# Performance work log

Measured on AMD Instinct MI355X. Metric: run time of the kernel, lower is better.

Reference implementation:

```python
import jax, jax.numpy as jnp
import numpy as np

# config constants (match init_kwargs)
T, B = 32, 32
H, W_IN, C_IN = 128, 128, 2
FH, FW = 32, 32
CF, CP = 64, 32
OUT = 128
PATCH = 8
TOPK_R = 4
KWTA = 16
SPARSITY = 0.5
BETA = 0.9
VTH = 1.0
EVT = 0.5
PH, PW = H // PATCH, W_IN // PATCH  # 16,16


def _topk_mask(x, k):
    # mask of entries >= k-th largest along last axis
    k = min(k, x.shape[-1])
    if k <= 0:
        return jnp.zeros_like(x)
    top_vals = jax.lax.top_k(x, k)[0]
    thresh = top_vals[..., k - 1:k]
    return (x >= thresh).astype(x.dtype)


def _block_sparse_mask(w, sparsity, block=4):
    h, wk, cin, cout = w.shape
    bh, bw = h // block, wk // block
    if bh == 0 or bw == 0:
        # 3x3 kernel with block=4 degenerates to a dense (all-ones) mask
        return jnp.ones((h, wk, 1, 1), dtype=w.dtype)
    core = w[:bh * block, :bw * block, :, :]
    blocks = core.reshape(bh, block, bw, block, cin, cout)
    scores = jnp.mean(jnp.abs(blocks), axis=(1, 3, 4, 5)).reshape(-1)
    keep = max(1, int(scores.shape[0] * (1.0 - sparsity)))
    gate = _topk_mask(scores[None, :], keep).reshape(bh, bw)
    gate = jnp.repeat(jnp.repeat(gate, block, axis=0), block, axis=1)
    mask = jnp.ones((h, wk), dtype=w.dtype).at[:bh * block, :bw * block].set(gate)
    return mask[:, :, None, None]


def _conv(x, w):
    return jax.lax.conv_general_dilated(
        x, w, (1, 1), 'SAME', dimension_numbers=('NHWC', 'HWIO', 'NHWC'))


@jax.custom_vjp
def _spike(v):
    return (v > 0).astype(v.dtype)

def _spike_fwd(v):
    return _spike(v), v

def _spike_bwd(v, g):
    # superspike surrogate gradient (k=25)
    return (g / (1.0 + 25.0 * jnp.abs(v)) ** 2,)

_spike.defvjp(_spike_fwd, _spike_bwd)


def setup_inputs() -> dict:
    key = jax.random.key(0)
    ks = jax.random.split(key, 8)
    def vs_uniform(k, shape):
        # VarianceScaling(1.0, fan_avg, uniform)
        fan_in = shape[0] * shape[1] * shape[2] if len(shape) == 4 else shape[0]
        fan_out = shape[0] * shape[1] * shape[3] if len(shape) == 4 else shape[1]
        limit = float(np.sqrt(3.0 / ((fan_in + fan_out) / 2.0)))
        return jax.random.uniform(k, shape, jnp.float32, -limit, limit)
    return {
        'x_seq': jax.random.normal(ks[0], (T, B, H, W_IN, C_IN), jnp.float32),
        'w_fovea': vs_uniform(ks[1], (3, 3, C_IN, CF)),
        'w_periph': vs_uniform(ks[2], (3, 3, C_IN, CP)),
        'head_w': vs_uniform(ks[3], (CF + CP, OUT)),
        'head_b': jnp.zeros((OUT,), jnp.float32),
        'route_w': vs_uniform(ks[4], (PH * PW, OUT)),
        'route_b': jnp.zeros((OUT,), jnp.float32),
    }


def reference(x_seq, w_fovea, w_periph, head_w, head_b, route_w, route_b):
    # block-sparse masks are constant across time: apply once
    w_f = w_fovea * _block_sparse_mask(w_fovea, SPARSITY)
    w_p = w_periph * _block_sparse_mask(w_periph, SPARSITY)

    def step(carry, x_t):
        vf, vp = carry
        event_mask = (jnp.abs(x_t) > EVT).astype(x_t.dtype)
        xs = x_t * event_mask
        # region activation router: mean |x| per patch
        patches = xs.reshape(B, PH, PATCH, PW, PATCH, C_IN)
        scores = jnp.mean(jnp.abs(patches), axis=(2, 4, 5)).reshape(B, PH * PW)
        region_gate = _topk_mask(scores, TOPK_R)
        # foveal crop around the best patch
        best = jnp.argmax(scores, axis=-1)
        cy = best // PW * PATCH + PATCH // 2
        cx = best % PW * PATCH + PATCH // 2
        y0 = jnp.clip(cy - FH // 2, 0, H - FH)
        x0 = jnp.clip(cx - FW // 2, 0, W_IN - FW)
        fovea = jax.vmap(
            lambda img, y, x: jax.lax.dynamic_slice(img, (y, x, 0), (FH, FW, C_IN))
        )(xs, y0, x0)
        # fovea conv + k-WTA channel gate
        ff = _conv(fovea, w_f)
        sal = jnp.mean(jnp.abs(ff), axis=(1, 2))            # (B, CF)
        channel_gate = _topk_mask(sal, KWTA)
        ff = ff * channel_gate[:, None, None, :]
        # periphery: half-res linear resize + conv
        periph = jax.image.resize(xs, (B, H // 2, W_IN // 2, C_IN), method='linear')
        pf = _conv(periph, w_p)
        # LIF updates (beta decay, threshold, soft reset)
        vf = BETA * vf + ff
        sf = _spike(vf - VTH)
        vf = vf - sf * VTH
        vp = BETA * vp + pf
        sp = _spike(vp - VTH)
        vp = vp - sp * VTH
        fused = jnp.concatenate([jnp.mean(sf, axis=(1, 2)), jnp.mean(sp, axis=(1, 2))], axis=-1)
        logits_t = fused @ head_w + head_b + scores @ route_w + route_b
        sr_t = jnp.stack([jnp.mean(sf), jnp.mean(sp)])
        active_ratio = jnp.mean(event_mask)
        route_stats = jnp.mean(region_gate, axis=0)
        chan_stats = jnp.mean(channel_gate, axis=0)
        return (vf, vp), (logits_t, sr_t, active_ratio, route_stats, chan_stats)

    vf0 = jnp.zeros((B, FH, FW, CF), x_seq.dtype)
    vp0 = jnp.zeros((B, H // 2, W_IN // 2, CP), x_seq.dtype)
    _, (logits_seq, sr_seq, active_seq, route_seq, chan_seq) = jax.lax.scan(
        step, (vf0, vp0), x_seq)
    out = jnp.mean(logits_seq, axis=0)  # readout='mean'
    return (out, logits_seq, jnp.mean(sr_seq, axis=0), jnp.mean(active_seq),
            jnp.mean(route_seq, axis=0), jnp.mean(chan_seq, axis=0))
```

## Files before the change

### kernel.cpp

```cpp
#include <hip/hip_runtime.h>

#define T_ 32
#define B_ 32
#define H_ 128
#define W_ 128
#define C_ 2
#define NP_ 256
#define CF_ 64
#define CP_ 32
#define OUT_ 128

#define PROW 136
#define PTB  8976
#define WTB  2312

#define OFF_LOGITS 4096
#define OFF_SR     135168
#define OFF_ACTIVE 135170
#define OFF_ROUTE  135171
#define OFF_CHAN   135427

#define CNT_N 323

typedef float f2 __attribute__((ext_vector_type(2)));

__device__ __forceinline__ float f4c(const float4& v, int i) {
  switch (i & 3) { case 0: return v.x; case 1: return v.y; case 2: return v.z; default: return v.w; }
}

__global__ void __launch_bounds__(256) k_pre(const float* __restrict__ x,
    const float* __restrict__ wf,
    float* __restrict__ scores_g, float* __restrict__ P, float* __restrict__ Wfbuf,
    float* __restrict__ chan_gate, unsigned* __restrict__ cnts) {
  const int tb = blockIdx.x, tid = threadIdx.x;
  __shared__ __align__(16) float xt[34*256];
  __shared__ float sm[NP_];
  __shared__ float salred[256];
  __shared__ float salv[64];
  __shared__ unsigned wsum[4];
  __shared__ int2 syx;
  const float* img = x + (size_t)tb*32768;
  unsigned cnt = 0;
  for (int chunk = 0; chunk < 4; ++chunk) {
    const int r0 = chunk*16;
    __syncthreads();
    for (int i4 = tid; i4 < 34*64; i4 += 256) {
      const int rr = i4 >> 6, off4 = i4 & 63;
      const int xr = 2*r0 - 1 + rr;
      float4 vv = make_float4(0.f, 0.f, 0.f, 0.f);
      if (xr >= 0 && xr < H_) {
        vv = *reinterpret_cast<const float4*>(img + (size_t)xr*256 + off4*4);
        if (rr >= 1 && rr <= 32) {
          cnt += (fabsf(vv.x) > 0.5f) + (fabsf(vv.y) > 0.5f)
               + (fabsf(vv.z) > 0.5f) + (fabsf(vv.w) > 0.5f);
        }
        vv.x = (fabsf(vv.x) > 0.5f) ? vv.x : 0.f;
        vv.y = (fabsf(vv.y) > 0.5f) ? vv.y : 0.f;
        vv.z = (fabsf(vv.z) > 0.5f) ? vv.z : 0.f;
        vv.w = (fabsf(vv.w) > 0.5f) ? vv.w : 0.f;
      }
      *reinterpret_cast<float4*>(&xt[i4*4]) = vv;
    }
    __syncthreads();
    {
      const int patch = tid >> 2, q = tid & 3;
      const int prl = patch >> 4, pc = patch & 15;
      const int row = 1 + prl*8 + q*2;
      float s = 0.f;
#pragma unroll
      for (int r2 = 0; r2 < 2; ++r2)
#pragma unroll
        for (int j = 0; j < 4; ++j) {
          const float4 vv = *reinterpret_cast<const float4*>(&xt[(row + r2)*256 + pc*16 + j*4]);
          s += fabsf(vv.x) + fabsf(vv.y) + fabsf(vv.z) + fabsf(vv.w);
        }
      s += __shfl_down(s, 1);
      s += __shfl_down(s, 2);
      if (q == 0) {
        const float sv = s * (1.f/128.f);
        sm[chunk*64 + patch] = sv;
        scores_g[tb*NP_ + chunk*64 + patch] = sv;
      }
    }
    float* Pt = P + (size_t)tb * PTB;
    if (tid < 128) {
      const int r = tid >> 3, rem = tid & 7;
      const int px4 = rem >> 1, ci = rem & 1;
      const int px = (px4 < 2) ? (px4 - 2) : (62 + px4);
      Pt[(r0 + r + 1)*PROW + (px + 2)*2 + ci] = 0.f;
    }
    if (chunk == 0 && tid < PROW) Pt[tid] = 0.f;
    if (chunk == 3 && tid < PROW) Pt[65*PROW + tid] = 0.f;
#pragma unroll
    for (int k = 0; k < 8; ++k) {
      const int idx = k*256 + tid;
      const int ci = idx & 1, rest = idx >> 1;
      const int col = rest & 63, row16 = rest >> 6;
      const int pr = r0 + row16;
      float wy0=0.125f, wy1=0.375f, wy2=0.375f, wy3=0.125f;
      if (pr == 0)       { wy0=0.f;     wy1=3.f/7.f; wy2=3.f/7.f; wy3=1.f/7.f; }
      else if (pr == 63) { wy0=1.f/7.f; wy1=3.f/7.f; wy2=3.f/7.f; wy3=0.f; }
      float wx0=0.125f, wx1=0.375f, wx2=0.375f, wx3=0.125f;
      if (col == 0)       { wx0=0.f;     wx1=3.f/7.f; wx2=3.f/7.f; wx3=1.f/7.f; }
      else if (col == 63) { wx0=1.f/7.f; wx1=3.f/7.f; wx2=3.f/7.f; wx3=0.f; }
      const int lr = 2*row16;
      const int cc0 = 2*col - 1;
      float val = 0.f;
#pragma unroll
      for (int j = 0; j < 4; ++j) {
        const float wyj = (j==0)?wy0:(j==1)?wy1:(j==2)?wy2:wy3;
        float h = 0.f;
#pragma unroll
        for (int i = 0; i < 4; ++i) {
          const float wxi = (i==0)?wx0:(i==1)?wx1:(i==2)?wx2:wx3;
          int cc = cc0 + i; cc = cc < 0 ? 0 : (cc > W_-1 ? W_-1 : cc);
          h += wxi * xt[(lr + j)*256 + cc*2 + ci];
        }
        val += wyj * h;
      }
      Pt[(pr + 1)*PROW + (col + 2)*2 + ci] = val;
    }
  }
  unsigned c64 = cnt;
#pragma unroll
  for (int off = 32; off > 0; off >>= 1) c64 += __shfl_down(c64, off);
  if ((tid & 63) == 0) wsum[tid >> 6] = c64;
  __syncthreads();
  if (tid == 0) atomicAdd(&cnts[0], wsum[0] + wsum[1] + wsum[2] + wsum[3]);
  {
    const float v = sm[tid];
    int cg = 0, eqb = 0;
    for (int q = 0; q < NP_; ++q) {
      cg  += (sm[q] > v) ? 1 : 0;
      eqb += ((sm[q] == v) && (q < tid)) ? 1 : 0;
    }
    if (cg < 4) atomicAdd(&cnts[1 + tid], 1u);
    if (cg == 0 && eqb == 0) {
      const int cy = (tid >> 4)*8 + 4, cx = (tid & 15)*8 + 4;
      int y0 = cy - 16; y0 = y0 < 0 ? 0 : (y0 > 96 ? 96 : y0);
      int x0 = cx - 16; x0 = x0 < 0 ? 0 : (x0 > 96 ? 96 : x0);
      syx = make_int2(y0, x0);
    }
  }
  float* tile = xt;
  for (int i = tid; i < 34*68; i += 256) tile[i] = 0.f;
  __syncthreads();
  const int2 yx = syx;
  {
    const int row = tid >> 3, seg = tid & 7;
    const float* src = img + (size_t)(yx.x + row)*256 + (yx.y + seg*4)*2;
    float4 a = *reinterpret_cast<const float4*>(src);
    float4 b4 = *reinterpret_cast<const float4*>(src + 4);
    a.x  = (fabsf(a.x)  > 0.5f) ? a.x  : 0.f;
    a.y  = (fabsf(a.y)  > 0.5f) ? a.y  : 0.f;
    a.z  = (fabsf(a.z)  > 0.5f) ? a.z  : 0.f;
    a.w  = (fabsf(a.w)  > 0.5f) ? a.w  : 0.f;
    b4.x = (fabsf(b4.x) > 0.5f) ? b4.x : 0.f;
    b4.y = (fabsf(b4.y) > 0.5f) ? b4.y : 0.f;
    b4.z = (fabsf(b4.z) > 0.5f) ? b4.z : 0.f;
    b4.w = (fabsf(b4.w) > 0.5f) ? b4.w : 0.f;
    float* dst = &tile[(row + 1)*68 + (seg*4 + 1)*2];
    *reinterpret_cast<float2*>(dst)     = make_float2(a.x, a.y);
    *reinterpret_cast<float2*>(dst + 2) = make_float2(a.z, a.w);
    *reinterpret_cast<float2*>(dst + 4) = make_float2(b4.x, b4.y);
    *reinterpret_cast<float2*>(dst + 6) = make_float2(b4.z, b4.w);
  }
  __syncthreads();
  {
    float* dst = Wfbuf + (size_t)tb*WTB;
    for (int i = tid; i < WTB/4; i += 256)
      *reinterpret_cast<float4*>(dst + i*4) = *reinterpret_cast<const float4*>(&tile[i*4]);
  }
  const int c = tid & 63, xg = tid >> 6;
  float wreg[18];
#pragma unroll
  for (int k = 0; k < 18; ++k) wreg[k] = wf[k*CF_ + c];
  const float* tbase = &tile[xg*16];
  float4 wb[3][5];
#pragma unroll
  for (int m = 0; m < 5; ++m) {
    wb[0][m] = *reinterpret_cast<const float4*>(tbase + m*4);
    wb[1][m] = *reinterpret_cast<const float4*>(tbase + 68 + m*4);
  }
  float sal = 0.f;
#pragma unroll
  for (int yy = 0; yy < 32; ++yy) {
#pragma unroll
    for (int m = 0; m < 5; ++m)
      wb[(yy+2)%3][m] = *reinterpret_cast<const float4*>(tbase + (yy+2)*68 + m*4);
#pragma unroll
    for (int k = 0; k < 8; ++k) {
      float acc = 0.f;
#pragma unroll
      for (int dy = 0; dy < 3; ++dy) {
#pragma unroll
        for (int dx = 0; dx < 3; ++dx) {
          const int r = k + dx;
          const float4 f = wb[(yy+dy)%3][r >> 1];
          acc += f4c(f, (r&1)*2)     * wreg[(dy*3+dx)*2]
               + f4c(f, (r&1)*2 + 1) * wreg[(dy*3+dx)*2 + 1];
        }
      }
      sal += fabsf(acc);
    }
  }
  salred[tid] = sal;
  __syncthreads();
  if (tid < 64)
    salv[tid] = (salred[tid] + salred[64+tid] + salred[128+tid] + salred[192+tid]) * (1.f/1024.f);
  __syncthreads();
  if (tid < 64) {
    const float sv = salv[tid];
    int cg = 0;
    for (int q = 0; q < 64; ++q) cg += (salv[q] > sv) ? 1 : 0;
    const float gate = (cg < 16) ? 1.f : 0.f;
    chan_gate[tb*CF_ + tid] = gate;
    if (gate > 0.f) atomicAdd(&cnts[257 + tid], 1u);
  }
}

__global__ void __launch_bounds__(256, 4) k_mem(const float* __restrict__ Wfbuf,
    const float* __restrict__ P, const float* __restrict__ wf, const float* __restrict__ wp,
    const float* __restrict__ chan_gate,
    unsigned* __restrict__ fov_part, unsigned* __restrict__ per_part) {
  const int tid = threadIdx.x;
  const int w = tid >> 6, l = tid & 63;
  if (blockIdx.x < 2048) {
    const int blk = blockIdx.x;
    const int b = blk >> 6, rem = blk & 63, cp = rem >> 1, half = rem & 1;
    const int ch0 = cp*2;
    const int row = half*16 + w*4 + (l >> 4);
    const int px0 = (l & 15)*2;
    f2 w01[18];
#pragma unroll
    for (int k = 0; k < 18; ++k) {
      f2 t_; t_.x = wf[k*CF_ + ch0]; t_.y = wf[k*CF_ + ch0 + 1];
      w01[k] = t_;
    }
    const float* p0 = Wfbuf + (size_t)b*WTB + (size_t)row*68 + px0*2;
    const float* gp = chan_gate + b*CF_ + ch0;
    const unsigned obase = (unsigned)((b*32 + cp)*8 + half*4 + w);
    f2 va = (f2)0.f, vb = (f2)0.f;
    float4 A[6], Bv[6];
    f2 gA, gB;
#pragma unroll
    for (int dy = 0; dy < 3; ++dy) {
      A[2*dy]   = *reinterpret_cast<const float4*>(p0 + dy*68);
      A[2*dy+1] = *reinterpret_cast<const float4*>(p0 + dy*68 + 4);
    }
    gA.x = gp[0]; gA.y = gp[1];
    for (int t = 0; t < T_; t += 2) {
      {
        const float* p1 = p0 + (size_t)(t + 1)*(B_*WTB);
#pragma unroll
        for (int dy = 0; dy < 3; ++dy) {
          Bv[2*dy]   = *reinterpret_cast<const float4*>(p1 + dy*68);
          Bv[2*dy+1] = *reinterpret_cast<const float4*>(p1 + dy*68 + 4);
        }
        gB.x = gp[(t + 1)*B_*CF_]; gB.y = gp[(t + 1)*B_*CF_ + 1];
      }
      {
        f2 aa = (f2)0.f, ab = (f2)0.f;
#pragma unroll
        for (int dy = 0; dy < 3; ++dy) {
          const float4 fa = A[2*dy], fb = A[2*dy+1];
          const f2 w0 = w01[dy*6], w0y = w01[dy*6+1], w1 = w01[dy*6+2],
                   w1y = w01[dy*6+3], w2 = w01[dy*6+4], w2y = w01[dy*6+5];
          aa += fa.x*w0 + fa.y*w0y + fa.z*w1 + fa.w*w1y + fb.x*w2 + fb.y*w2y;
          ab += fa.z*w0 + fa.w*w0y + fb.x*w1 + fb.y*w1y + fb.z*w2 + fb.w*w2y;
        }
        f2 na = 0.9f*va + aa*gA;
        f2 nb = 0.9f*vb + ab*gA;
        const bool s0a = na.x > 1.f, s1a = na.y > 1.f, s0b = nb.x > 1.f, s1b = nb.y > 1.f;
        va.x = s0a ? na.x - 1.f : na.x;  va.y = s1a ? na.y - 1.f : na.y;
        vb.x = s0b ? nb.x - 1.f : nb.x;  vb.y = s1b ? nb.y - 1.f : nb.y;
        const unsigned packed =
            (unsigned)(__popcll(__ballot(s0a)) + __popcll(__ballot(s0b)))
          | ((unsigned)(__popcll(__ballot(s1a)) + __popcll(__ballot(s1b))) << 16);
        if (l == 0) fov_part[obase + (unsigned)t*8192u] = packed;
      }
      if (t + 2 < T_) {
        const float* p2 = p0 + (size_t)(t + 2)*(B_*WTB);
#pragma unroll
        for (int dy = 0; dy < 3; ++dy) {
          A[2*dy]   = *reinterpret_cast<const float4*>(p2 + dy*68);
          A[2*dy+1] = *reinterpret_cast<const float4*>(p2 + dy*68 + 4);
        }
        gA.x = gp[(t + 2)*B_*CF_]; gA.y = gp[(t + 2)*B_*CF_ + 1];
      }
      {
        f2 aa = (f2)0.f, ab = (f2)0.f;
#pragma unroll
        for (int dy = 0; dy < 3; ++dy) {
          const float4 fa = Bv[2*dy], fb = Bv[2*dy+1];
          const f2 w0 = w01[dy*6], w0y = w01[dy*6+1], w1 = w01[dy*6+2],
                   w1y = w01[dy*6+3], w2 = w01[dy*6+4], w2y = w01[dy*6+5];
          aa += fa.x*w0 + fa.y*w0y + fa.z*w1 + fa.w*w1y + fb.x*w2 + fb.y*w2y;
          ab += fa.z*w0 + fa.w*w0y + fb.x*w1 + fb.y*w1y + fb.z*w2 + fb.w*w2y;
        }
        f2 na = 0.9f*va + aa*gB;
        f2 nb = 0.9f*vb + ab*gB;
        const bool s0a = na.x > 1.f, s1a = na.y > 1.f, s0b = nb.x > 1.f, s1b = nb.y > 1.f;
        va.x = s0a ? na.x - 1.f : na.x;  va.y = s1a ? na.y - 1.f : na.y;
        vb.x = s0b ? nb.x - 1.f : nb.x;  vb.y = s1b ? nb.y - 1.f : nb.y;
        const unsigned packed =
            (unsigned)(__popcll(__ballot(s0a)) + __popcll(__ballot(s0b)))
          | ((unsigned)(__popcll(__ballot(s1a)) + __popcll(__ballot(s1b))) << 16);
        if (l == 0) fov_part[obase + (unsigned)(t + 1)*8192u] = packed;
      }
    }
  } else {
    const int blk = blockIdx.x - 2048;
    const int b = blk >> 7, rem = blk & 127, cp = rem >> 3, rq = rem & 7;
    const int ch0 = cp*2;
    const int row = rq*8 + w*2 + (l >> 5);
    const int px0 = (l & 31)*2;
    f2 w01[18];
#pragma unroll
    for (int k = 0; k < 18; ++k) {
      f2 t_; t_.x = wp[k*CP_ + ch0]; t_.y = wp[k*CP_ + ch0 + 1];
      w01[k] = t_;
    }
    const float* p0 = P + (size_t)b*PTB + (size_t)row*PROW + px0*2;
    const unsigned obase = (unsigned)((b*16 + cp)*32 + rq*4 + w);
    f2 va = (f2)0.f, vb = (f2)0.f;
    float4 A[9], Bv[9];
#pragma unroll
    for (int dy = 0; dy < 3; ++dy) {
      A[3*dy]   = *reinterpret_cast<const float4*>(p0 + dy*PROW);
      A[3*dy+1] = *reinterpret_cast<const float4*>(p0 + dy*PROW + 4);
      A[3*dy+2] = *reinterpret_cast<const float4*>(p0 + dy*PROW + 8);
    }
    for (int t = 0; t < T_; t += 2) {
      {
        const float* p1 = p0 + (size_t)(t + 1)*PTB*B_;
#pragma unroll
        for (int dy = 0; dy < 3; ++dy) {
          Bv[3*dy]   = *reinterpret_cast<const float4*>(p1 + dy*PROW);
          Bv[3*dy+1] = *reinterpret_cast<const float4*>(p1 + dy*PROW + 4);
          Bv[3*dy+2] = *reinterpret_cast<const float4*>(p1 + dy*PROW + 8);
        }
      }
      {
        f2 aa = (f2)0.f, ab = (f2)0.f;
#pragma unroll
        for (int dy = 0; dy < 3; ++dy) {
          const float4 f0 = A[3*dy], f1 = A[3*dy+1], f2v = A[3*dy+2];
          const f2 w0 = w01[dy*6], w0y = w01[dy*6+1], w1 = w01[dy*6+2],
                   w1y = w01[dy*6+3], w2 = w01[dy*6+4], w2y = w01[dy*6+5];
          aa += f0.z*w0 + f0.w*w0y + f1.x*w1 + f1.y*w1y + f1.z*w2 + f1.w*w2y;
          ab += f1.x*w0 + f1.y*w0y + f1.z*w1 + f1.w*w1y + f2v.x*w2 + f2v.y*w2y;
        }
        f2 na = 0.9f*va + aa;
        f2 nb = 0.9f*vb + ab;
        const bool s0a = na.x > 1.f, s1a = na.y > 1.f, s0b = nb.x > 1.f, s1b = nb.y > 1.f;
        va.x = s0a ? na.x - 1.f : na.x;  va.y = s1a ? na.y - 1.f : na.y;
        vb.x = s0b ? nb.x - 1.f : nb.x;  vb.y = s1b ? nb.y - 1.f : nb.y;
        const unsigned packed =
            (unsigned)(__popcll(__ballot(s0a)) + __popcll(__ballot(s0b)))
          | ((unsigned)(__popcll(__ballot(s1a)) + __popcll(__ballot(s1b))) << 16);
        if (l == 0) per_part[obase + (unsigned)t*16384u] = packed;
      }
      if (t + 2 < T_) {
        const float* p2 = p0 + (size_t)(t + 2)*PTB*B_;
#pragma unroll
        for (int dy = 0; dy < 3; ++dy) {
          A[3*dy]   = *reinterpret_cast<const float4*>(p2 + dy*PROW);
          A[3*dy+1] = *reinterpret_cast<const float4*>(p2 + dy*PROW + 4);
          A[3*dy+2] = *reinterpret_cast<const float4*>(p2 + dy*PROW + 8);
        }
      }
      {
        f2 aa = (f2)0.f, ab = (f2)0.f;
#pragma unroll
        for (int dy = 0; dy < 3; ++dy) {
          const float4 f0 = Bv[3*dy], f1 = Bv[3*dy+1], f2v = Bv[3*dy+2];
          const f2 w0 = w01[dy*6], w0y = w01[dy*6+1], w1 = w01[dy*6+2],
                   w1y = w01[dy*6+3], w2 = w01[dy*6+4], w2y = w01[dy*6+5];
          aa += f0.z*w0 + f0.w*w0y + f1.x*w1 + f1.y*w1y + f1.z*w2 + f1.w*w2y;
          ab += f1.x*w0 + f1.y*w0y + f1.z*w1 + f1.w*w1y + f2v.x*w2 + f2v.y*w2y;
        }
        f2 na = 0.9f*va + aa;
        f2 nb = 0.9f*vb + ab;
        const bool s0a = na.x > 1.f, s1a = na.y > 1.f, s0b = nb.x > 1.f, s1b = nb.y > 1.f;
        va.x = s0a ? na.x - 1.f : na.x;  va.y = s1a ? na.y - 1.f : na.y;
        vb.x = s0b ? nb.x - 1.f : nb.x;  vb.y = s1b ? nb.y - 1.f : nb.y;
        const unsigned packed =
            (unsigned)(__popcll(__ballot(s0a)) + __popcll(__ballot(s0b)))
          | ((unsigned)(__popcll(__ballot(s1a)) + __popcll(__ballot(s1b))) << 16);
        if (l == 0) per_part[obase + (unsigned)(t + 1)*16384u] = packed;
      }
    }
  }
}

__global__ void __launch_bounds__(256) k_logits(const float* __restrict__ scores,
    const unsigned* __restrict__ fov_part, const unsigned* __restrict__ per_part,
    const float* __restrict__ head_w, const float* __restrict__ head_b,
    const float* __restrict__ route_w, const float* __restrict__ route_b,
    float* __restrict__ logits, unsigned* __restrict__ tot) {
  const int tb = blockIdx.x, tid = threadIdx.x;
  __shared__ float sc[NP_];
  __shared__ float fu[96];
  sc[tid] = scores[tb*NP_ + tid];
  if (tid < 64) {
    const unsigned* fp = fov_part + (size_t)tb*256;
    const int cp = tid >> 1, sh = (tid & 1)*16;
    unsigned fsum = 0;
#pragma unroll
    for (int i = 0; i < 8; ++i) fsum += (fp[cp*8 + i] >> sh) & 0xFFFFu;
    fu[tid] = (float)fsum * (1.f/1024.f);
    unsigned r = fsum;
#pragma unroll
    for (int off = 32; off > 0; off >>= 1) r += __shfl_down(r, off);
    if (tid == 0) atomicAdd(&tot[0], r);
  } else if (tid < 128) {
    const int c = tid - 64;
    unsigned psum = 0;
    if (c < 32) {
      const unsigned* pp = per_part + (size_t)tb*512;
      const int cp = c >> 1, sh = (c & 1)*16;
#pragma unroll 8
      for (int i = 0; i < 32; ++i) psum += (pp[cp*32 + i] >> sh) & 0xFFFFu;
      fu[64 + c] = (float)psum * (1.f/4096.f);
    }
    unsigned r = psum;
#pragma unroll
    for (int off = 32; off > 0; off >>= 1) r += __shfl_down(r, off);
    if (tid == 64) atomicAdd(&tot[1], r);
  }
  __syncthreads();
  if (tid < 128) {
    const int o = tid;
    float acc = head_b[o] + route_b[o];
#pragma unroll 8
    for (int k = 0; k < 96; ++k)  acc += fu[k]*head_w[k*OUT_ + o];
#pragma unroll 8
    for (int p = 0; p < NP_; ++p) acc += sc[p]*route_w[p*OUT_ + o];
    logits[tb*OUT_ + o] = acc;
  }
}

__global__ void __launch_bounds__(256) k_final(const float* __restrict__ logits,
    float* __restrict__ dout, const unsigned* __restrict__ cnts) {
  const int blk = blockIdx.x, tid = threadIdx.x;
  if (blk < 16) {
    const int idx = blk*256 + tid;
    const int b = idx >> 7, o = idx & 127;
    float s = 0.f;
#pragma unroll
    for (int t = 0; t < T_; ++t) s += logits[(t*B_ + b)*OUT_ + o];
    dout[idx] = s * (1.f/32.f);
  } else {
    if (tid == 0) {
      dout[OFF_SR]     = (float)cnts[321] * (1.f/67108864.f);
      dout[OFF_SR + 1] = (float)cnts[322] * (1.f/134217728.f);
      dout[OFF_ACTIVE] = (float)cnts[0]   * (1.f/33554432.f);
    }
    dout[OFF_ROUTE + tid] = (float)cnts[1 + tid] * (1.f/1024.f);
    if (tid < 64) dout[OFF_CHAN + tid] = (float)cnts[257 + tid] * (1.f/1024.f);
  }
}

extern "C" void kernel_launch(void* const* d_in, const int* in_sizes, int n_in,
                              void* d_out, int out_size, void* d_ws, size_t ws_size,
                              hipStream_t stream) {
  const float* x       = (const float*)d_in[0];
  const float* wf      = (const float*)d_in[1];
  const float* wp      = (const float*)d_in[2];
  const float* head_w  = (const float*)d_in[3];
  const float* head_b  = (const float*)d_in[4];
  const float* route_w = (const float*)d_in[5];
  const float* route_b = (const float*)d_in[6];
  float* out = (float*)d_out;

  float*    ws_P      = (float*)d_ws;
  float*    ws_Wf     = ws_P + (size_t)1024*PTB;
  float*    ws_scores = ws_Wf + (size_t)1024*WTB;
  float*    ws_gate   = ws_scores + T_*B_*NP_;
  unsigned* fov_part  = (unsigned*)(ws_gate + T_*B_*CF_);
  unsigned* per_part  = fov_part + (size_t)T_*B_*256;
  unsigned* ws_cnt    = per_part + (size_t)T_*B_*512;

  hipMemsetAsync(ws_cnt, 0, CNT_N*sizeof(unsigned), stream);

  k_pre   <<<T_*B_, 256, 0, stream>>>(x, wf, ws_scores, ws_P, ws_Wf, ws_gate, ws_cnt);
  k_mem   <<<6144,  256, 0, stream>>>(ws_Wf, ws_P, wf, wp, ws_gate, fov_part, per_part);
  k_logits<<<T_*B_, 256, 0, stream>>>(ws_scores, fov_part, per_part, head_w, head_b,
                                      route_w, route_b, out + OFF_LOGITS, ws_cnt + 321);
  k_final <<<17, 256, 0, stream>>>(out + OFF_LOGITS, out, ws_cnt);
}
```

Baseline: 272.5 us.

## Stage conv input tiles in double-buffered LDS instead of per-thread global loads

The fovea and periphery LIF conv loops in k_mem now load each timestep's input tile cooperatively into a double-buffered shared-memory array. Previously every thread fetched its own overlapping 3-row stencil straight from global memory. The next timestep is prefetched into registers and written to the other LDS buffer after compute, with one barrier per step. This removes redundant global loads of overlapping halo rows, at the cost of a __syncthreads per timestep and about 10.9 KB of LDS per block, which could limit occupancy.

```diff
diff --git a/kernel.cpp b/kernel.cpp
--- a/kernel.cpp
+++ b/kernel.cpp
@@ -223,173 +223,123 @@
     const float* __restrict__ P, const float* __restrict__ wf, const float* __restrict__ wp,
     const float* __restrict__ chan_gate,
     unsigned* __restrict__ fov_part, unsigned* __restrict__ per_part) {
+  __shared__ __align__(16) float lds[2*1360];
   const int tid = threadIdx.x;
   const int w = tid >> 6, l = tid & 63;
   if (blockIdx.x < 2048) {
     const int blk = blockIdx.x;
     const int b = blk >> 6, rem = blk & 63, cp = rem >> 1, half = rem & 1;
     const int ch0 = cp*2;
-    const int row = half*16 + w*4 + (l >> 4);
-    const int px0 = (l & 15)*2;
+    const int brow = w*4 + (l >> 4);
+    const int po = (l & 15)*4;
     f2 w01[18];
 #pragma unroll
     for (int k = 0; k < 18; ++k) {
       f2 t_; t_.x = wf[k*CF_ + ch0]; t_.y = wf[k*CF_ + ch0 + 1];
       w01[k] = t_;
     }
-    const float* p0 = Wfbuf + (size_t)b*WTB + (size_t)row*68 + px0*2;
+    const float* gsrc = Wfbuf + (size_t)b*WTB + half*16*68;
     const float* gp = chan_gate + b*CF_ + ch0;
     const unsigned obase = (unsigned)((b*32 + cp)*8 + half*4 + w);
     f2 va = (f2)0.f, vb = (f2)0.f;
-    float4 A[6], Bv[6];
-    f2 gA, gB;
-#pragma unroll
-    for (int dy = 0; dy < 3; ++dy) {
-      A[2*dy]   = *reinterpret_cast<const float4*>(p0 + dy*68);
-      A[2*dy+1] = *reinterpret_cast<const float4*>(p0 + dy*68 + 4);
-    }
-    gA.x = gp[0]; gA.y = gp[1];
-    for (int t = 0; t < T_; t += 2) {
-      {
-        const float* p1 = p0 + (size_t)(t + 1)*(B_*WTB);
-#pragma unroll
-        for (int dy = 0; dy < 3; ++dy) {
-          Bv[2*dy]   = *reinterpret_cast<const float4*>(p1 + dy*68);
-          Bv[2*dy+1] = *reinterpret_cast<const float4*>(p1 + dy*68 + 4);
-        }
-        gB.x = gp[(t + 1)*B_*CF_]; gB.y = gp[(t + 1)*B_*CF_ + 1];
-      }
-      {
-        f2 aa = (f2)0.f, ab = (f2)0.f;
-#pragma unroll
-        for (int dy = 0; dy < 3; ++dy) {
-          const float4 fa = A[2*dy], fb = A[2*dy+1];
-          const f2 w0 = w01[dy*6], w0y = w01[dy*6+1], w1 = w01[dy*6+2],
-                   w1y = w01[dy*6+3], w2 = w01[dy*6+4], w2y = w01[dy*6+5];
-          aa += fa.x*w0 + fa.y*w0y + fa.z*w1 + fa.w*w1y + fb.x*w2 + fb.y*w2y;
-          ab += fa.z*w0 + fa.w*w0y + fb.x*w1 + fb.y*w1y + fb.z*w2 + fb.w*w2y;
-        }
-        f2 na = 0.9f*va + aa*gA;
-        f2 nb = 0.9f*vb + ab*gA;
-        const bool s0a = na.x > 1.f, s1a = na.y > 1.f, s0b = nb.x > 1.f, s1b = nb.y > 1.f;
-        va.x = s0a ? na.x - 1.f : na.x;  va.y = s1a ? na.y - 1.f : na.y;
-        vb.x = s0b ? nb.x - 1.f : nb.x;  vb.y = s1b ? nb.y - 1.f : nb.y;
-        const unsigned packed =
-            (unsigned)(__popcll(__ballot(s0a)) + __popcll(__ballot(s0b)))
-          | ((unsigned)(__popcll(__ballot(s1a)) + __popcll(__ballot(s1b))) << 16);
-        if (l == 0) fov_part[obase + (unsigned)t*8192u] = packed;
-      }
-      if (t + 2 < T_) {
-        const float* p2 = p0 + (size_t)(t + 2)*(B_*WTB);
-#pragma unroll
-        for (int dy = 0; dy < 3; ++dy) {
-          A[2*dy]   = *reinterpret_cast<const float4*>(p2 + dy*68);
-          A[2*dy+1] = *reinterpret_cast<const float4*>(p2 + dy*68 + 4);
-        }
-        gA.x = gp[(t + 2)*B_*CF_]; gA.y = gp[(t + 2)*B_*CF_ + 1];
-      }
-      {
-        f2 aa = (f2)0.f, ab = (f2)0.f;
-#pragma unroll
-        for (int dy = 0; dy < 3; ++dy) {
-          const float4 fa = Bv[2*dy], fb = Bv[2*dy+1];
-          const f2 w0 = w01[dy*6], w0y = w01[dy*6+1], w1 = w01[dy*6+2],
-                   w1y = w01[dy*6+3], w2 = w01[dy*6+4], w2y = w01[dy*6+5];
-          aa += fa.x*w0 + fa.y*w0y + fa.z*w1 + fa.w*w1y + fb.x*w2 + fb.y*w2y;
-          ab += fa.z*w0 + fa.w*w0y + fb.x*w1 + fb.y*w1y + fb.z*w2 + fb.w*w2y;
-        }
-        f2 na = 0.9f*va + aa*gB;
-        f2 nb = 0.9f*vb + ab*gB;
-        const bool s0a = na.x > 1.f, s1a = na.y > 1.f, s0b = nb.x > 1.f, s1b = nb.y > 1.f;
-        va.x = s0a ? na.x - 1.f : na.x;  va.y = s1a ? na.y - 1.f : na.y;
-        vb.x = s0b ? nb.x - 1.f : nb.x;  vb.y = s1b ? nb.y - 1.f : nb.y;
-        const unsigned packed =
-            (unsigned)(__popcll(__ballot(s0a)) + __popcll(__ballot(s0b)))
-          | ((unsigned)(__popcll(__ballot(s1a)) + __popcll(__ballot(s1b))) << 16);
-        if (l == 0) fov_part[obase + (unsigned)(t + 1)*8192u] = packed;
-      }
+    float4 r0, r1;
+    r0 = *reinterpret_cast<const float4*>(gsrc + tid*4);
+    if (tid < 50) r1 = *reinterpret_cast<const float4*>(gsrc + (tid + 256)*4);
+    *reinterpret_cast<float4*>(&lds[tid*4]) = r0;
+    if (tid < 50) *reinterpret_cast<float4*>(&lds[(tid + 256)*4]) = r1;
+    int cur = 0;
+    for (int t = 0; t < T_; ++t) {
+      __syncthreads();
+      if (t + 1 < T_) {
+        const float* gn = gsrc + (size_t)(t + 1)*(B_*WTB);
+        r0 = *reinterpret_cast<const float4*>(gn + tid*4);
+        if (tid < 50) r1 = *reinterpret_cast<const float4*>(gn + (tid + 256)*4);
+      }
+      __builtin_amdgcn_sched_barrier(0);
+      f2 g; g.x = gp[(size_t)t*B_*CF_]; g.y = gp[(size_t)t*B_*CF_ + 1];
+      const float* Lb = &lds[cur*1360];
+      f2 aa = (f2)0.f, ab = (f2)0.f;
+#pragma unroll
+      for (int dy = 0; dy < 3; ++dy) {
+        const float4 fa = *reinterpret_cast<const float4*>(Lb + (brow + dy)*68 + po);
+        const float4 fb = *reinterpret_cast<const float4*>(Lb + (brow + dy)*68 + po + 4);
+        const f2 w0 = w01[dy*6], w0y = w01[dy*6+1], w1 = w01[dy*6+2],
+                 w1y = w01[dy*6+3], w2 = w01[dy*6+4], w2y = w01[dy*6+5];
+        aa += fa.x*w0 + fa.y*w0y + fa.z*w1 + fa.w*w1y + fb.x*w2 + fb.y*w2y;
+        ab += fa.z*w0 + fa.w*w0y + fb.x*w1 + fb.y*w1y + fb.z*w2 + fb.w*w2y;
+      }
+      f2 na = 0.9f*va + aa*g;
+      f2 nb = 0.9f*vb + ab*g;
+      const bool s0a = na.x > 1.f, s1a = na.y > 1.f, s0b = nb.x > 1.f, s1b = nb.y > 1.f;
+      va.x = s0a ? na.x - 1.f : na.x;  va.y = s1a ? na.y - 1.f : na.y;
+      vb.x = s0b ? nb.x - 1.f : nb.x;  vb.y = s1b ? nb.y - 1.f : nb.y;
+      const unsigned packed =
+          (unsigned)(__popcll(__ballot(s0a)) + __popcll(__ballot(s0b)))
+        | ((unsigned)(__popcll(__ballot(s1a)) + __popcll(__ballot(s1b))) << 16);
+      if (l == 0) fov_part[obase + (unsigned)t*8192u] = packed;
+      if (t + 1 < T_) {
+        float* Lw = &lds[(cur ^ 1)*1360];
+        *reinterpret_cast<float4*>(Lw + tid*4) = r0;
+        if (tid < 50) *reinterpret_cast<float4*>(Lw + (tid + 256)*4) = r1;
+      }
+      cur ^= 1;
     }
   } else {
     const int blk = blockIdx.x - 2048;
     const int b = blk >> 7, rem = blk & 127, cp = rem >> 3, rq = rem & 7;
     const int ch0 = cp*2;
-    const int row = rq*8 + w*2 + (l >> 5);
-    const int px0 = (l & 31)*2;
+    const int brow = w*2 + (l >> 5);
+    const int po = (l & 31)*4;
     f2 w01[18];
 #pragma unroll
     for (int k = 0; k < 18; ++k) {
       f2 t_; t_.x = wp[k*CP_ + ch0]; t_.y = wp[k*CP_ + ch0 + 1];
       w01[k] = t_;
     }
-    const float* p0 = P + (size_t)b*PTB + (size_t)row*PROW + px0*2;
+    const float* gsrc = P + (size_t)b*PTB + rq*8*PROW;
     const unsigned obase = (unsigned)((b*16 + cp)*32 + rq*4 + w);
     f2 va = (f2)0.f, vb = (f2)0.f;
-    float4 A[9], Bv[9];
-#pragma unroll
-    for (int dy = 0; dy < 3; ++dy) {
-      A[3*dy]   = *reinterpret_cast<const float4*>(p0 + dy*PROW);
-      A[3*dy+1] = *reinterpret_cast<const float4*>(p0 + dy*PROW + 4);
-      A[3*dy+2] = *reinterpret_cast<const float4*>(p0 + dy*PROW + 8);
-    }
-    for (int t = 0; t < T_; t += 2) {
-      {
-        const float* p1 = p0 + (size_t)(t + 1)*PTB*B_;
-#pragma unroll
-        for (int dy = 0; dy < 3; ++dy) {
-          Bv[3*dy]   = *reinterpret_cast<const float4*>(p1 + dy*PROW);
-          Bv[3*dy+1] = *reinterpret_cast<const float4*>(p1 + dy*PROW + 4);
-          Bv[3*dy+2] = *reinterpret_cast<const float4*>(p1 + dy*PROW + 8);
-        }
-      }
-      {
-        f2 aa = (f2)0.f, ab = (f2)0.f;
-#pragma unroll
-        for (int dy = 0; dy < 3; ++dy) {
-          const float4 f0 = A[3*dy], f1 = A[3*dy+1], f2v = A[3*dy+2];
-          const f2 w0 = w01[dy*6], w0y = w01[dy*6+1], w1 = w01[dy*6+2],
-                   w1y = w01[dy*6+3], w2 = w01[dy*6+4], w2y = w01[dy*6+5];
-          aa += f0.z*w0 + f0.w*w0y + f1.x*w1 + f1.y*w1y + f1.z*w2 + f1.w*w2y;
-          ab += f1.x*w0 + f1.y*w0y + f1.z*w1 + f1.w*w1y + f2v.x*w2 + f2v.y*w2y;
-        }
-        f2 na = 0.9f*va + aa;
-        f2 nb = 0.9f*vb + ab;
-        const bool s0a = na.x > 1.f, s1a = na.y > 1.f, s0b = nb.x > 1.f, s1b = nb.y > 1.f;
-        va.x = s0a ? na.x - 1.f : na.x;  va.y = s1a ? na.y - 1.f : na.y;
-        vb.x = s0b ? nb.x - 1.f : nb.x;  vb.y = s1b ? nb.y - 1.f : nb.y;
-        const unsigned packed =
-            (unsigned)(__popcll(__ballot(s0a)) + __popcll(__ballot(s0b)))
-          | ((unsigned)(__popcll(__ballot(s1a)) + __popcll(__ballot(s1b))) << 16);
-        if (l == 0) per_part[obase + (unsigned)t*16384u] = packed;
-      }
-      if (t + 2 < T_) {
-        const float* p2 = p0 + (size_t)(t + 2)*PTB*B_;
-#pragma unroll
-        for (int dy = 0; dy < 3; ++dy) {
-          A[3*dy]   = *reinterpret_cast<const float4*>(p2 + dy*PROW);
-          A[3*dy+1] = *reinterpret_cast<const float4*>(p2 + dy*PROW + 4);
-          A[3*dy+2] = *reinterpret_cast<const float4*>(p2 + dy*PROW + 8);
-        }
-      }
-      {
-        f2 aa = (f2)0.f, ab = (f2)0.f;
-#pragma unroll
-        for (int dy = 0; dy < 3; ++dy) {
-          const float4 f0 = Bv[3*dy], f1 = Bv[3*dy+1], f2v = Bv[3*dy+2];
-          const f2 w0 = w01[dy*6], w0y = w01[dy*6+1], w1 = w01[dy*6+2],
-                   w1y = w01[dy*6+3], w2 = w01[dy*6+4], w2y = w01[dy*6+5];
-          aa += f0.z*w0 + f0.w*w0y + f1.x*w1 + f1.y*w1y + f1.z*w2 + f1.w*w2y;
-          ab += f1.x*w0 + f1.y*w0y + f1.z*w1 + f1.w*w1y + f2v.x*w2 + f2v.y*w2y;
-        }
-        f2 na = 0.9f*va + aa;
-        f2 nb = 0.9f*vb + ab;
-        const bool s0a = na.x > 1.f, s1a = na.y > 1.f, s0b = nb.x > 1.f, s1b = nb.y > 1.f;
-        va.x = s0a ? na.x - 1.f : na.x;  va.y = s1a ? na.y - 1.f : na.y;
-        vb.x = s0b ? nb.x - 1.f : nb.x;  vb.y = s1b ? nb.y - 1.f : nb.y;
-        const unsigned packed =
-            (unsigned)(__popcll(__ballot(s0a)) + __popcll(__ballot(s0b)))
-          | ((unsigned)(__popcll(__ballot(s1a)) + __popcll(__ballot(s1b))) << 16);
-        if (l == 0) per_part[obase + (unsigned)(t + 1)*16384u] = packed;
-      }
+    float4 r0, r1;
+    r0 = *reinterpret_cast<const float4*>(gsrc + tid*4);
+    if (tid < 84) r1 = *reinterpret_cast<const float4*>(gsrc + (tid + 256)*4);
+    *reinterpret_cast<float4*>(&lds[tid*4]) = r0;
+    if (tid < 84) *reinterpret_cast<float4*>(&lds[(tid + 256)*4]) = r1;
+    int cur = 0;
+    for (int t = 0; t < T_; ++t) {
+      __syncthreads();
+      if (t + 1 < T_) {
+        const float* gn = gsrc + (size_t)(t + 1)*(B_*PTB);
+        r0 = *reinterpret_cast<const float4*>(gn + tid*4);
+        if (tid < 84) r1 = *reinterpret_cast<const float4*>(gn + (tid + 256)*4);
+      }
+      __builtin_amdgcn_sched_barrier(0);
+      const float* Lb = &lds[cur*1360];
+      f2 aa = (f2)0.f, ab = (f2)0.f;
+#pragma unroll
+      for (int dy = 0; dy < 3; ++dy) {
+        const float4 f0 = *reinterpret_cast<const float4*>(Lb + (brow + dy)*136 + po);
+        const float4 f1 = *reinterpret_cast<const float4*>(Lb + (brow + dy)*136 + po + 4);
+        const float4 f2v = *reinterpret_cast<const float4*>(Lb + (brow + dy)*136 + po + 8);
+        const f2 w0 = w01[dy*6], w0y = w01[dy*6+1], w1 = w01[dy*6+2],
+                 w1y = w01[dy*6+3], w2 = w01[dy*6+4], w2y = w01[dy*6+5];
+        aa += f0.z*w0 + f0.w*w0y + f1.x*w1 + f1.y*w1y + f1.z*w2 + f1.w*w2y;
+        ab += f1.x*w0 + f1.y*w0y + f1.z*w1 + f1.w*w1y + f2v.x*w2 + f2v.y*w2y;
+      }
+      f2 na = 0.9f*va + aa;
+      f2 nb = 0.9f*vb + ab;
+      const bool s0a = na.x > 1.f, s1a = na.y > 1.f, s0b = nb.x > 1.f, s1b = nb.y > 1.f;
+      va.x = s0a ? na.x - 1.f : na.x;  va.y = s1a ? na.y - 1.f : na.y;
+      vb.x = s0b ? nb.x - 1.f : nb.x;  vb.y = s1b ? nb.y - 1.f : nb.y;
+      const unsigned packed =
+          (unsigned)(__popcll(__ballot(s0a)) + __popcll(__ballot(s0b)))
+        | ((unsigned)(__popcll(__ballot(s1a)) + __popcll(__ballot(s1b))) << 16);
+      if (l == 0) per_part[obase + (unsigned)t*16384u] = packed;
+      if (t + 1 < T_) {
+        float* Lw = &lds[(cur ^ 1)*1360];
+        *reinterpret_cast<float4*>(Lw + tid*4) = r0;
+        if (tid < 84) *reinterpret_cast<float4*>(Lw + (tid + 256)*4) = r1;
+      }
+      cur ^= 1;
     }
   }
 }
```

Measured after the change: 277.7 us. No clear change (+1.9%).
